# Performance work log

Hardware: AMD Instinct MI355X
Metric: run time of the kernel (lower is better)

Reference implementation:

```python
import jax, jax.numpy as jnp
import numpy as np

N_NODES = 100000
N_EDGES = 1600000
IN_CH = 128
HID = 64
HEADS = 2
OUT_CH = 2
EDGE_DIM = 3
NEG_SLOPE = 0.2
EPS = 1e-16  # PyG softmax denominator epsilon


def gat_conv(x, edge_index, edge_attr, W, We, att_src, att_dst, att_edge, bias, heads, out_ch, concat):
    """Faithful PyG GATConv (edge_dim enabled, eval mode, add_self_loops handled by caller=False here
    since the repo passes raw edge_index; PyG default add_self_loops=True is intentionally mirrored below)."""
    N = x.shape[0]
    src, dst = edge_index[0], edge_index[1]
    H, C = heads, out_ch
    h = (x @ W).reshape(N, H, C)                    # [N,H,C] node projections
    e = (edge_attr @ We).reshape(-1, H, C)          # [E,H,C] edge projections
    a_src = jnp.sum(h * att_src, axis=-1)           # [N,H]
    a_dst = jnp.sum(h * att_dst, axis=-1)           # [N,H]
    alpha = a_src[src] + a_dst[dst] + jnp.sum(e * att_edge, axis=-1)  # [E,H]
    alpha = jax.nn.leaky_relu(alpha, NEG_SLOPE)
    # segment softmax over incoming edges of each dst node
    amax = jax.ops.segment_max(alpha, dst, num_segments=N)            # [N,H]
    amax = jnp.where(jnp.isfinite(amax), amax, 0.0)
    alpha = jnp.exp(alpha - amax[dst])
    denom = jax.ops.segment_sum(alpha, dst, num_segments=N)           # [N,H]
    alpha = alpha / (denom[dst] + EPS)
    msg = h[src] * alpha[:, :, None]                                  # [E,H,C]
    out = jax.ops.segment_sum(msg, dst, num_segments=N)               # [N,H,C]
    if concat:
        out = out.reshape(N, H * C)
    else:
        out = out.mean(axis=1)
    return out + bias


def add_self_loops(edge_index, edge_attr, n):
    loops = jnp.arange(n, dtype=edge_index.dtype)
    ei = jnp.concatenate([edge_index, jnp.stack([loops, loops])], axis=1)
    ea = jnp.concatenate([edge_attr, jnp.zeros((n, edge_attr.shape[1]), edge_attr.dtype)], axis=0)
    return ei, ea


def setup_inputs() -> dict:
    key = jax.random.key(0)
    ks = jax.random.split(key, 16)
    s = 0.1
    x = jax.random.normal(ks[0], (N_NODES, IN_CH), jnp.float32)
    edge_index = jax.random.randint(ks[1], (2, N_EDGES), 0, N_NODES, jnp.int64 if jax.config.jax_enable_x64 else jnp.int32)
    edge_feat = jax.random.normal(ks[2], (N_EDGES, EDGE_DIM), jnp.float32)
    HC = HEADS * HID
    return {
        "x": x, "edge_index": edge_index, "edge_feat": edge_feat,
        "W1": jax.random.normal(ks[3], (IN_CH, HC), jnp.float32) * s,
        "We1": jax.random.normal(ks[4], (EDGE_DIM, HC), jnp.float32) * s,
        "as1": jax.random.normal(ks[5], (1, HEADS, HID), jnp.float32) * s,
        "ad1": jax.random.normal(ks[6], (1, HEADS, HID), jnp.float32) * s,
        "ae1": jax.random.normal(ks[7], (1, HEADS, HID), jnp.float32) * s,
        "b1": jnp.zeros((HC,), jnp.float32),
        "W2": jax.random.normal(ks[8], (HC, OUT_CH), jnp.float32) * s,
        "We2": jax.random.normal(ks[9], (EDGE_DIM, OUT_CH), jnp.float32) * s,
        "as2": jax.random.normal(ks[10], (1, 1, OUT_CH), jnp.float32) * s,
        "ad2": jax.random.normal(ks[11], (1, 1, OUT_CH), jnp.float32) * s,
        "ae2": jax.random.normal(ks[12], (1, 1, OUT_CH), jnp.float32) * s,
        "b2": jnp.zeros((OUT_CH,), jnp.float32),
    }


def reference(x, edge_index, edge_feat, W1, We1, as1, ad1, ae1, b1, W2, We2, as2, ad2, ae2, b2):
    # eval mode: F.dropout is identity
    ei, ea = add_self_loops(edge_index, edge_feat, x.shape[0])  # PyG GATConv default add_self_loops=True
    h = gat_conv(x, ei, ea, W1, We1, as1, ad1, ae1, b1, HEADS, HID, concat=True)
    h = jax.nn.elu(h)
    out = gat_conv(h, ei, ea, W2, We2, as2, ad2, ae2, b2, 1, OUT_CH, concat=False)
    return out
```

## Files before the change

### kernel.cpp

```cpp
#include <hip/hip_runtime.h>
#include <hip/hip_bf16.h>

#define NN 100000
#define NE 1600000
#define NEG_SLOPE 0.2f
#define GEPS 1e-16f
#define WSHIFT 4.0f

#define HB 32
#define EB (NE / HB)
#define HPASS 4
#define HBIN 25000
#define HBW (HBIN / 2)

typedef __attribute__((ext_vector_type(8))) short short8;
typedef __attribute__((ext_vector_type(4))) float f32x4;
typedef __attribute__((ext_vector_type(2))) _Float16 h2v;

__device__ __forceinline__ unsigned short f2b(float f) {
  unsigned u = __float_as_uint(f);
  u += 0x7fffu + ((u >> 16) & 1u);
  return (unsigned short)(u >> 16);
}
__device__ __forceinline__ unsigned short f2h(float f) {
  _Float16 h = (_Float16)f;
  return __builtin_bit_cast(unsigned short, h);
}
__device__ __forceinline__ unsigned pkh2(float lo, float hi) {
  return (unsigned)f2h(lo) | ((unsigned)f2h(hi) << 16);
}
__device__ __forceinline__ float dot2h(unsigned a, unsigned b, float c) {
  return __builtin_amdgcn_fdot2(__builtin_bit_cast(h2v, a), __builtin_bit_cast(h2v, b), c, false);
}
__device__ __forceinline__ unsigned permb(unsigned s0, unsigned s1, int sel) {
  return __builtin_amdgcn_perm(s0, s1, sel);
}
#define HSEL_LO 0x05040100
#define HSEL_HI 0x07060302
#define ONE2    0x3C003C00u

__global__ void k_prep(const float* __restrict__ We1, const float* __restrict__ ae1,
                       const float* __restrict__ We2, const float* __restrict__ ae2,
                       const float* __restrict__ W1, const float* __restrict__ as1,
                       const float* __restrict__ ad1,
                       float* __restrict__ q, float4* __restrict__ pq) {
  int t = threadIdx.x;
  if (t < 6) {
    int d = t >> 1, hh = t & 1;
    float s = 0.f;
    for (int c = 0; c < 64; ++c) s += We1[d * 128 + hh * 64 + c] * ae1[hh * 64 + c];
    q[t] = s;
  } else if (t < 9) {
    int d = t - 6;
    q[8 + d] = We2[d * 2 + 0] * ae2[0] + We2[d * 2 + 1] * ae2[1];
  }
  if (t < 128) {
    float s0 = 0.f, s1 = 0.f, d0 = 0.f, d1 = 0.f;
    for (int c = 0; c < 64; ++c) {
      float w0 = W1[t * 128 + c], w1 = W1[t * 128 + 64 + c];
      s0 += w0 * as1[c];      s1 += w1 * as1[64 + c];
      d0 += w0 * ad1[c];      d1 += w1 * ad1[64 + c];
    }
    pq[t] = make_float4(s0, s1, d0, d1);
  }
}

__global__ __launch_bounds__(512, 4) void k_gemm(const float* __restrict__ x,
                                                 const float* __restrict__ W,
                                                 const float4* __restrict__ pq,
                                                 unsigned short* __restrict__ h1b,
                                                 float* __restrict__ a1s,
                                                 float* __restrict__ a1d) {
  __shared__ unsigned short xa[128 * 128];
  __shared__ unsigned short wt[128 * 128];
  int t = threadIdx.x;
  int row0 = blockIdx.x * 128;

  {
    int kr = t >> 2, n0 = (t & 3) * 32;
    const float* wp = &W[kr * 128 + n0];
    int cb = kr >> 3, klo = kr & 7;
#pragma unroll
    for (int j = 0; j < 8; ++j) {
      float4 v = *(const float4*)&wp[j * 4];
      int n = n0 + j * 4;
      wt[(n + 0) * 128 + ((cb ^ ((n + 0) & 15)) * 8) + klo] = f2b(v.x);
      wt[(n + 1) * 128 + ((cb ^ ((n + 1) & 15)) * 8) + klo] = f2b(v.y);
      wt[(n + 2) * 128 + ((cb ^ ((n + 2) & 15)) * 8) + klo] = f2b(v.z);
      wt[(n + 3) * 128 + ((cb ^ ((n + 3) & 15)) * 8) + klo] = f2b(v.w);
    }
  }
  {
    int lrow = t >> 2, qq = t & 3;
    int grow = row0 + lrow; if (grow >= NN) grow = NN - 1;
    const float* xp = &x[(size_t)grow * 128 + qq * 32];
    const float4* pqp = &pq[qq * 32];
    float ps0 = 0.f, ps1 = 0.f, pd0 = 0.f, pd1 = 0.f;
    int sw = lrow & 15;
#pragma unroll
    for (int j = 0; j < 4; ++j) {
      float4 u = *(const float4*)&xp[j * 8];
      float4 v = *(const float4*)&xp[j * 8 + 4];
      float xs[8] = {u.x, u.y, u.z, u.w, v.x, v.y, v.z, v.w};
      short8 sv;
#pragma unroll
      for (int e = 0; e < 8; ++e) {
        float4 pv = pqp[j * 8 + e];
        ps0 += xs[e] * pv.x; ps1 += xs[e] * pv.y;
        pd0 += xs[e] * pv.z; pd1 += xs[e] * pv.w;
        sv[e] = (short)f2b(xs[e]);
      }
      int c = qq * 4 + j;
      *(short8*)&xa[lrow * 128 + ((c ^ sw) * 8)] = sv;
    }
    ps0 += __shfl_xor(ps0, 1); ps0 += __shfl_xor(ps0, 2);
    ps1 += __shfl_xor(ps1, 1); ps1 += __shfl_xor(ps1, 2);
    pd0 += __shfl_xor(pd0, 1); pd0 += __shfl_xor(pd0, 2);
    pd1 += __shfl_xor(pd1, 1); pd1 += __shfl_xor(pd1, 2);
    if (qq == 0) {
      *(float2*)&a1s[grow * 2] = make_float2(ps0, ps1);
      *(float2*)&a1d[grow * 2] = make_float2(pd0, pd1);
    }
  }
  __syncthreads();

  int lane = t & 63, w = t >> 6;
  int m = lane & 15, quad = lane >> 4;
  int wm = (w & 1) * 64, wn = (w >> 1) * 32;
  f32x4 acc[4][2];
#pragma unroll
  for (int mi = 0; mi < 4; ++mi)
#pragma unroll
    for (int ni = 0; ni < 2; ++ni) acc[mi][ni] = (f32x4)(0.f);

#pragma unroll
  for (int kk = 0; kk < 4; ++kk) {
    int c = kk * 4 + quad;
    int co = (c ^ m) * 8;
    short8 a[4], b[2];
#pragma unroll
    for (int mi = 0; mi < 4; ++mi)
      a[mi] = *(const short8*)&xa[(wm + mi * 16 + m) * 128 + co];
#pragma unroll
    for (int ni = 0; ni < 2; ++ni)
      b[ni] = *(const short8*)&wt[(wn + ni * 16 + m) * 128 + co];
#pragma unroll
    for (int mi = 0; mi < 4; ++mi)
#pragma unroll
      for (int ni = 0; ni < 2; ++ni)
        acc[mi][ni] = __builtin_amdgcn_mfma_f32_16x16x32_bf16(a[mi], b[ni], acc[mi][ni], 0, 0, 0);
  }
#pragma unroll
  for (int mi = 0; mi < 4; ++mi)
#pragma unroll
    for (int r = 0; r < 4; ++r) {
      int grow = row0 + wm + mi * 16 + quad * 4 + r;
      if (grow >= NN) grow = NN - 1;
#pragma unroll
      for (int ni = 0; ni < 2; ++ni)
        h1b[(size_t)grow * 128 + wn + ni * 16 + m] = f2h(acc[mi][ni][r]);
    }
}

__global__ __launch_bounds__(1024) void k_hist(const int* __restrict__ ei,
                                               unsigned short* __restrict__ off16,
                                               unsigned short* __restrict__ rank) {
  __shared__ unsigned cnt[HBW];
  int b = blockIdx.x >> 2;
  int pass = blockIdx.x & 3;
  int base = pass * HBIN;
  int t = threadIdx.x;
  for (int i = t; i < HBW; i += 1024) cnt[i] = 0;
  __syncthreads();
  const int* dsts = &ei[NE + b * EB];
  for (int i = t * 4; i < EB; i += 4096) {
    int4 d = *(const int4*)&dsts[i];
    int dv[4] = {d.x, d.y, d.z, d.w};
#pragma unroll
    for (int j = 0; j < 4; ++j) {
      int rel = dv[j] - base;
      if ((unsigned)rel < (unsigned)HBIN) {
        unsigned sh = (unsigned)(rel & 1) << 4;
        unsigned old = atomicAdd(&cnt[rel >> 1], 1u << sh);
        rank[b * EB + i + j] = (unsigned short)((old >> sh) & 0xffffu);
      }
    }
  }
  __syncthreads();
  unsigned short* dp = &off16[(size_t)b * NN + base];
  for (int i = t; i < HBW; i += 1024) *(unsigned*)&dp[i * 2] = cnt[i];
}

__global__ void k_sumdeg(unsigned short* __restrict__ off16, int* __restrict__ deg) {
  int n = blockIdx.x * 256 + threadIdx.x;
  if (n >= NN) return;
  int run = 0;
#pragma unroll
  for (int b = 0; b < HB; ++b) {
    size_t idx = (size_t)b * NN + n;
    int c = off16[idx];
    off16[idx] = (unsigned short)run;
    run += c;
  }
  deg[n] = run;
}

__device__ __forceinline__ int padlen(int d) { return (d + 8) & ~7; }

__global__ void k_scan1(const int* __restrict__ deg, int* __restrict__ bsum) {
  __shared__ int lds[256];
  int t = threadIdx.x;
  int base = blockIdx.x * 1024 + t * 4;
  int s = 0;
  for (int j = 0; j < 4; ++j) { int i = base + j; s += (i < NN) ? padlen(deg[i]) : 0; }
  lds[t] = s; __syncthreads();
  for (int o = 128; o > 0; o >>= 1) { if (t < o) lds[t] += lds[t + o]; __syncthreads(); }
  if (t == 0) bsum[blockIdx.x] = lds[0];
}

__global__ void k_scan2(int* __restrict__ bsum, int nb) {
  __shared__ int lds[128];
  int t = threadIdx.x;
  int v = (t < nb) ? bsum[t] : 0;
  lds[t] = v; __syncthreads();
  for (int o = 1; o < 128; o <<= 1) {
    int u = (t >= o) ? lds[t - o] : 0;
    __syncthreads();
    lds[t] += u;
    __syncthreads();
  }
  if (t < nb) bsum[t] = lds[t] - v;
}

__global__ void k_scan3(const int* __restrict__ deg, const int* __restrict__ bbase,
                        const float* __restrict__ a1s, const float* __restrict__ a1d,
                        int* __restrict__ rowptr, float4* __restrict__ cpk) {
  __shared__ int lds[256];
  int t = threadIdx.x;
  int base = blockIdx.x * 1024 + t * 4;
  int v[4]; int s = 0;
  for (int j = 0; j < 4; ++j) { int i = base + j; v[j] = (i < NN) ? padlen(deg[i]) : 0; s += v[j]; }
  lds[t] = s; __syncthreads();
  for (int o = 1; o < 256; o <<= 1) {
    int u = (t >= o) ? lds[t - o] : 0;
    __syncthreads();
    lds[t] += u;
    __syncthreads();
  }
  int excl = lds[t] - s + bbase[blockIdx.x];
  for (int j = 0; j < 4; ++j) {
    int i = base + j;
    if (i <= NN) rowptr[i] = excl;
    if (i < NN) {
      float al0 = a1s[i * 2] + a1d[i * 2];
      float al1 = a1s[i * 2 + 1] + a1d[i * 2 + 1];
      al0 = al0 > 0.f ? al0 : NEG_SLOPE * al0;
      al1 = al1 > 0.f ? al1 : NEG_SLOPE * al1;
      float4 pk;
      pk.x = __uint_as_float(pkh2(__expf(al0 - WSHIFT), __expf(al1 - WSHIFT)));
      pk.y = 0.f; pk.z = __int_as_float(i); pk.w = 0.f;
      cpk[excl] = pk;
      float4 pad;
      pad.x = 0.f; pad.y = -1e30f; pad.z = __int_as_float(i); pad.w = 0.f;
      for (int k = 1 + deg[i]; k < v[j]; ++k) cpk[excl + k] = pad;
    }
    excl += v[j];
  }
}

__global__ void k_scatter(const int* __restrict__ ei, const float* __restrict__ ef,
                          const float* __restrict__ a1s, const float* __restrict__ a1d,
                          const float* __restrict__ q, const int* __restrict__ rowptr,
                          const unsigned short* __restrict__ rank,
                          const unsigned short* __restrict__ off16,
                          float4* __restrict__ cpk) {
  int t4 = blockIdx.x * 256 + threadIdx.x;
  if (t4 >= NE / 4) return;
  int e0 = t4 * 4;
  int hb = e0 / EB;
  const unsigned short* offp = &off16[(size_t)hb * NN];
  int4 ss = *(const int4*)&ei[e0];
  int4 dd = *(const int4*)&ei[NE + e0];
  ushort4 rk = *(const ushort4*)&rank[e0];
  float4 fA = *(const float4*)&ef[e0 * 3];
  float4 fB = *(const float4*)&ef[e0 * 3 + 4];
  float4 fC = *(const float4*)&ef[e0 * 3 + 8];
  float f[4][3] = {{fA.x, fA.y, fA.z}, {fA.w, fB.x, fB.y},
                   {fB.z, fB.w, fC.x}, {fC.y, fC.z, fC.w}};
  int src[4] = {ss.x, ss.y, ss.z, ss.w};
  int dst[4] = {dd.x, dd.y, dd.z, dd.w};
  int rnk[4] = {rk.x, rk.y, rk.z, rk.w};
#pragma unroll
  for (int j = 0; j < 4; ++j) {
    float e0h = f[j][0] * q[0] + f[j][1] * q[2] + f[j][2] * q[4];
    float e1h = f[j][0] * q[1] + f[j][1] * q[3] + f[j][2] * q[5];
    float ez  = f[j][0] * q[8] + f[j][1] * q[9] + f[j][2] * q[10];
    float al0 = a1s[src[j] * 2] + a1d[dst[j] * 2] + e0h;
    float al1 = a1s[src[j] * 2 + 1] + a1d[dst[j] * 2 + 1] + e1h;
    al0 = al0 > 0.f ? al0 : NEG_SLOPE * al0;
    al1 = al1 > 0.f ? al1 : NEG_SLOPE * al1;
    int pos = rowptr[dst[j]] + 1 + (int)offp[dst[j]] + rnk[j];
    float4 pk;
    pk.x = __uint_as_float(pkh2(__expf(al0 - WSHIFT), __expf(al1 - WSHIFT)));
    pk.y = ez; pk.z = __int_as_float(src[j]); pk.w = 0.f;
    cpk[pos] = pk;
  }
}

__global__ __launch_bounds__(256) void k_agg1(const unsigned short* __restrict__ h1b,
                                              const int* __restrict__ rowptr,
                                              const float4* __restrict__ cpk,
                                              const float* __restrict__ b1,
                                              const float* __restrict__ W2,
                                              const float* __restrict__ as2,
                                              const float* __restrict__ ad2,
                                              float4* __restrict__ nd) {
  int n = (int)((blockIdx.x * 256 + threadIdx.x) >> 6);
  int lane = threadIdx.x & 63;
  if (n >= NN) return;
  int s0 = rowptr[n], s1 = rowptr[n + 1];
  int g = lane >> 4;
  int lp = lane & 15;
  int wsel = (lp >= 8) ? HSEL_HI : HSEL_LO;

  float acc[8];
#pragma unroll
  for (int j = 0; j < 8; ++j) acc[j] = 0.f;
  float den = 0.f;

  int i = s0;
  for (; i + 16 <= s1; i += 16) {
    float4 pA = cpk[i + g], pB = cpk[i + 4 + g], pC = cpk[i + 8 + g], pD = cpk[i + 12 + g];
    uint4 vA = *((const uint4*)(h1b + ((size_t)__float_as_int(pA.z) << 7)) + lp);
    uint4 vB = *((const uint4*)(h1b + ((size_t)__float_as_int(pB.z) << 7)) + lp);
    uint4 vC = *((const uint4*)(h1b + ((size_t)__float_as_int(pC.z) << 7)) + lp);
    uint4 vD = *((const uint4*)(h1b + ((size_t)__float_as_int(pD.z) << 7)) + lp);
    unsigned wAB = permb(__float_as_uint(pB.x), __float_as_uint(pA.x), wsel);
    unsigned wCD = permb(__float_as_uint(pD.x), __float_as_uint(pC.x), wsel);
    den = dot2h(wAB, ONE2, den);
    den = dot2h(wCD, ONE2, den);
    acc[0] = dot2h(permb(vB.x, vA.x, HSEL_LO), wAB, acc[0]);
    acc[1] = dot2h(permb(vB.x, vA.x, HSEL_HI), wAB, acc[1]);
    acc[2] = dot2h(permb(vB.y, vA.y, HSEL_LO), wAB, acc[2]);
    acc[3] = dot2h(permb(vB.y, vA.y, HSEL_HI), wAB, acc[3]);
    acc[4] = dot2h(permb(vB.z, vA.z, HSEL_LO), wAB, acc[4]);
    acc[5] = dot2h(permb(vB.z, vA.z, HSEL_HI), wAB, acc[5]);
    acc[6] = dot2h(permb(vB.w, vA.w, HSEL_LO), wAB, acc[6]);
    acc[7] = dot2h(permb(vB.w, vA.w, HSEL_HI), wAB, acc[7]);
    acc[0] = dot2h(permb(vD.x, vC.x, HSEL_LO), wCD, acc[0]);
    acc[1] = dot2h(permb(vD.x, vC.x, HSEL_HI), wCD, acc[1]);
    acc[2] = dot2h(permb(vD.y, vC.y, HSEL_LO), wCD, acc[2]);
    acc[3] = dot2h(permb(vD.y, vC.y, HSEL_HI), wCD, acc[3]);
    acc[4] = dot2h(permb(vD.z, vC.z, HSEL_LO), wCD, acc[4]);
    acc[5] = dot2h(permb(vD.z, vC.z, HSEL_HI), wCD, acc[5]);
    acc[6] = dot2h(permb(vD.w, vC.w, HSEL_LO), wCD, acc[6]);
    acc[7] = dot2h(permb(vD.w, vC.w, HSEL_HI), wCD, acc[7]);
  }
  if (i < s1) {
    float4 pA = cpk[i + g], pB = cpk[i + 4 + g];
    uint4 vA = *((const uint4*)(h1b + ((size_t)__float_as_int(pA.z) << 7)) + lp);
    uint4 vB = *((const uint4*)(h1b + ((size_t)__float_as_int(pB.z) << 7)) + lp);
    unsigned wAB = permb(__float_as_uint(pB.x), __float_as_uint(pA.x), wsel);
    den = dot2h(wAB, ONE2, den);
    acc[0] = dot2h(permb(vB.x, vA.x, HSEL_LO), wAB, acc[0]);
    acc[1] = dot2h(permb(vB.x, vA.x, HSEL_HI), wAB, acc[1]);
    acc[2] = dot2h(permb(vB.y, vA.y, HSEL_LO), wAB, acc[2]);
    acc[3] = dot2h(permb(vB.y, vA.y, HSEL_HI), wAB, acc[3]);
    acc[4] = dot2h(permb(vB.z, vA.z, HSEL_LO), wAB, acc[4]);
    acc[5] = dot2h(permb(vB.z, vA.z, HSEL_HI), wAB, acc[5]);
    acc[6] = dot2h(permb(vB.w, vA.w, HSEL_LO), wAB, acc[6]);
    acc[7] = dot2h(permb(vB.w, vA.w, HSEL_HI), wAB, acc[7]);
  }
#pragma unroll
  for (int o = 16; o <= 32; o <<= 1) {
    den += __shfl_xor(den, o);
#pragma unroll
    for (int j = 0; j < 8; ++j) acc[j] += __shfl_xor(acc[j], o);
  }
  float4 bA = *(const float4*)&b1[lp * 8];
  float4 bB = *(const float4*)&b1[lp * 8 + 4];
  float bb[8] = {bA.x, bA.y, bA.z, bA.w, bB.x, bB.y, bB.z, bB.w};
  float inv = 1.f / (den + GEPS);
  float r[8];
#pragma unroll
  for (int j = 0; j < 8; ++j) {
    float v = acc[j] * inv + bb[j];
    r[j] = v > 0.f ? v : __expf(v) - 1.f;
  }
  float4 wA = *(const float4*)&W2[lp * 16];
  float4 wB = *(const float4*)&W2[lp * 16 + 4];
  float4 wC = *(const float4*)&W2[lp * 16 + 8];
  float4 wD = *(const float4*)&W2[lp * 16 + 12];
  float p20 = r[0] * wA.x + r[1] * wA.z + r[2] * wB.x + r[3] * wB.z
            + r[4] * wC.x + r[5] * wC.z + r[6] * wD.x + r[7] * wD.z;
  float p21 = r[0] * wA.y + r[1] * wA.w + r[2] * wB.y + r[3] * wB.w
            + r[4] * wC.y + r[5] * wC.w + r[6] * wD.y + r[7] * wD.w;
#pragma unroll
  for (int o = 1; o <= 8; o <<= 1) { p20 += __shfl_xor(p20, o); p21 += __shfl_xor(p21, o); }
  if (lane == 0) {
    float4 v;
    v.x = p20; v.y = p21;
    v.z = p20 * as2[0] + p21 * as2[1];
    v.w = p20 * ad2[0] + p21 * ad2[1];
    nd[n] = v;
  }
}

__global__ __launch_bounds__(256) void k_agg2(const int* __restrict__ rowptr,
                                              const float4* __restrict__ cpk,
                                              const float4* __restrict__ nd,
                                              const float* __restrict__ b2,
                                              float* __restrict__ out) {
  int wid = (int)((blockIdx.x * 256 + threadIdx.x) >> 6);
  int lane = threadIdx.x & 63;
  int g = lane >> 4, lp = lane & 15;
  int n = wid * 4 + g;
  if (n >= NN) return;
  int s0 = rowptr[n], s1 = rowptr[n + 1];
  float adn = nd[n].w;
  float den = 0.f, acc0 = 0.f, acc1 = 0.f;
  for (int i = s0 + lp; i < s1; i += 16) {
    float4 pk = cpk[i];
    int s = __float_as_int(pk.z);
    float4 ns = nd[s];
    float v = ns.z + adn + pk.y;
    v = v > 0.f ? v : NEG_SLOPE * v;
    float p = __expf(v);
    den += p;
    acc0 += p * ns.x;
    acc1 += p * ns.y;
  }
#pragma unroll
  for (int o = 1; o <= 8; o <<= 1) {
    den += __shfl_xor(den, o);
    acc0 += __shfl_xor(acc0, o);
    acc1 += __shfl_xor(acc1, o);
  }
  if (lp == 0) {
    float2 r;
    r.x = acc0 / (den + GEPS) + b2[0];
    r.y = acc1 / (den + GEPS) + b2[1];
    *(float2*)&out[n * 2] = r;
  }
}

extern "C" void kernel_launch(void* const* d_in, const int* in_sizes, int n_in,
                              void* d_out, int out_size, void* d_ws, size_t ws_size,
                              hipStream_t stream) {
  (void)in_sizes; (void)n_in; (void)out_size; (void)ws_size;
  const float* x   = (const float*)d_in[0];
  const int*   ei  = (const int*)d_in[1];
  const float* ef  = (const float*)d_in[2];
  const float* W1  = (const float*)d_in[3];
  const float* We1 = (const float*)d_in[4];
  const float* as1 = (const float*)d_in[5];
  const float* ad1 = (const float*)d_in[6];
  const float* ae1 = (const float*)d_in[7];
  const float* b1  = (const float*)d_in[8];
  const float* W2  = (const float*)d_in[9];
  const float* We2 = (const float*)d_in[10];
  const float* as2 = (const float*)d_in[11];
  const float* ad2 = (const float*)d_in[12];
  const float* ae2 = (const float*)d_in[13];
  const float* b2  = (const float*)d_in[14];
  float* out = (float*)d_out;

  char* w = (char*)d_ws;
  auto alloc = [&](size_t bytes) -> char* {
    char* p = w; w += (bytes + 255) & ~(size_t)255; return p;
  };
  unsigned short* h1b = (unsigned short*)alloc((size_t)NN * 128 * 2);
  float*  a1s    = (float*)alloc((size_t)NN * 2 * 4);
  float*  a1d    = (float*)alloc((size_t)NN * 2 * 4);
  float4* nd     = (float4*)alloc((size_t)NN * 16);
  float*  q      = (float*)alloc(64);
  float4* pq     = (float4*)alloc(128 * 16);
  int*    deg    = (int*)alloc((size_t)NN * 4);
  int*    rowptr = (int*)alloc((size_t)(NN + 1) * 4);
  unsigned short* rank  = (unsigned short*)alloc((size_t)NE * 2);
  unsigned short* off16 = (unsigned short*)alloc((size_t)HB * NN * 2);
  int*    bsum   = (int*)alloc(128 * 4);
  float4* cpk    = (float4*)alloc(((size_t)NE + 8 * NN) * 16);

  const int NB_SCAN = (NN + 1023) / 1024;

  hipLaunchKernelGGL(k_prep, dim3(1), dim3(128), 0, stream,
                     We1, ae1, We2, ae2, W1, as1, ad1, q, pq);
  hipLaunchKernelGGL(k_gemm, dim3((NN + 127) / 128), dim3(512), 0, stream,
                     x, W1, pq, h1b, a1s, a1d);
  hipLaunchKernelGGL(k_hist, dim3(HB * HPASS), dim3(1024), 0, stream, ei, off16, rank);
  hipLaunchKernelGGL(k_sumdeg, dim3((NN + 255) / 256), dim3(256), 0, stream, off16, deg);
  hipLaunchKernelGGL(k_scan1, dim3(NB_SCAN), dim3(256), 0, stream, deg, bsum);
  hipLaunchKernelGGL(k_scan2, dim3(1), dim3(128), 0, stream, bsum, NB_SCAN);
  hipLaunchKernelGGL(k_scan3, dim3(NB_SCAN), dim3(256), 0, stream,
                     deg, bsum, a1s, a1d, rowptr, cpk);
  hipLaunchKernelGGL(k_scatter, dim3((NE / 4 + 255) / 256), dim3(256), 0, stream,
                     ei, ef, a1s, a1d, q, rowptr, rank, off16, cpk);
  hipLaunchKernelGGL(k_agg1, dim3((NN * 64 + 255) / 256), dim3(256), 0, stream,
                     h1b, rowptr, cpk, b1, W2, as2, ad2, nd);
  hipLaunchKernelGGL(k_agg2, dim3(((NN + 3) / 4 * 64 + 255) / 256), dim3(256), 0, stream,
                     rowptr, cpk, nd, b2, out);
}
```

Baseline: 347.8 us.

## Scatter edge permutation then build compact CSR payload in a sequential pass

The scatter step now writes only a 4-byte edge index into the padded CSR order. A new k_build kernel walks that order sequentially and computes attention weights into an 8-byte (weight, src) array plus a separate edge-logit array. This replaces the 16-byte random scatter writes with small scattered writes followed by coalesced gathers, and shrinks the payload k_agg1 reads per edge from 16 to 8 bytes. It adds one kernel launch and random reads of ei/ef/a1s/a1d in the build pass, and reuses the rank/off16 buffer memory for the edge-logit array.

```diff
diff --git a/kernel.cpp b/kernel.cpp
--- a/kernel.cpp
+++ b/kernel.cpp
@@ -12,6 +12,10 @@
 #define HPASS 4
 #define HBIN 25000
 #define HBW (HBIN / 2)
+#define CAPS (NE + 8 * NN)
+
+#define PM_PAD  0xFFFFFFFFu
+#define PM_SELF 0x40000000u
 
 typedef __attribute__((ext_vector_type(8))) short short8;
 typedef __attribute__((ext_vector_type(4))) float f32x4;
@@ -233,8 +237,7 @@
 }
 
 __global__ void k_scan3(const int* __restrict__ deg, const int* __restrict__ bbase,
-                        const float* __restrict__ a1s, const float* __restrict__ a1d,
-                        int* __restrict__ rowptr, float4* __restrict__ cpk) {
+                        int* __restrict__ rowptr, unsigned* __restrict__ perm) {
   __shared__ int lds[256];
   int t = threadIdx.x;
   int base = blockIdx.x * 1024 + t * 4;
@@ -252,64 +255,91 @@
     int i = base + j;
     if (i <= NN) rowptr[i] = excl;
     if (i < NN) {
-      float al0 = a1s[i * 2] + a1d[i * 2];
-      float al1 = a1s[i * 2 + 1] + a1d[i * 2 + 1];
-      al0 = al0 > 0.f ? al0 : NEG_SLOPE * al0;
-      al1 = al1 > 0.f ? al1 : NEG_SLOPE * al1;
-      float4 pk;
-      pk.x = __uint_as_float(pkh2(__expf(al0 - WSHIFT), __expf(al1 - WSHIFT)));
-      pk.y = 0.f; pk.z = __int_as_float(i); pk.w = 0.f;
-      cpk[excl] = pk;
-      float4 pad;
-      pad.x = 0.f; pad.y = -1e30f; pad.z = __int_as_float(i); pad.w = 0.f;
-      for (int k = 1 + deg[i]; k < v[j]; ++k) cpk[excl + k] = pad;
+      perm[excl] = PM_SELF | (unsigned)i;
+      for (int k = 1 + deg[i]; k < v[j]; ++k) perm[excl + k] = PM_PAD;
     }
     excl += v[j];
   }
 }
 
-__global__ void k_scatter(const int* __restrict__ ei, const float* __restrict__ ef,
-                          const float* __restrict__ a1s, const float* __restrict__ a1d,
-                          const float* __restrict__ q, const int* __restrict__ rowptr,
-                          const unsigned short* __restrict__ rank,
-                          const unsigned short* __restrict__ off16,
-                          float4* __restrict__ cpk) {
+__global__ void k_pscat(const int* __restrict__ ei, const int* __restrict__ rowptr,
+                        const unsigned short* __restrict__ rank,
+                        const unsigned short* __restrict__ off16,
+                        unsigned* __restrict__ perm) {
   int t4 = blockIdx.x * 256 + threadIdx.x;
   if (t4 >= NE / 4) return;
   int e0 = t4 * 4;
   int hb = e0 / EB;
   const unsigned short* offp = &off16[(size_t)hb * NN];
-  int4 ss = *(const int4*)&ei[e0];
   int4 dd = *(const int4*)&ei[NE + e0];
   ushort4 rk = *(const ushort4*)&rank[e0];
-  float4 fA = *(const float4*)&ef[e0 * 3];
-  float4 fB = *(const float4*)&ef[e0 * 3 + 4];
-  float4 fC = *(const float4*)&ef[e0 * 3 + 8];
-  float f[4][3] = {{fA.x, fA.y, fA.z}, {fA.w, fB.x, fB.y},
-                   {fB.z, fB.w, fC.x}, {fC.y, fC.z, fC.w}};
-  int src[4] = {ss.x, ss.y, ss.z, ss.w};
   int dst[4] = {dd.x, dd.y, dd.z, dd.w};
   int rnk[4] = {rk.x, rk.y, rk.z, rk.w};
 #pragma unroll
   for (int j = 0; j < 4; ++j) {
-    float e0h = f[j][0] * q[0] + f[j][1] * q[2] + f[j][2] * q[4];
-    float e1h = f[j][0] * q[1] + f[j][1] * q[3] + f[j][2] * q[5];
-    float ez  = f[j][0] * q[8] + f[j][1] * q[9] + f[j][2] * q[10];
-    float al0 = a1s[src[j] * 2] + a1d[dst[j] * 2] + e0h;
-    float al1 = a1s[src[j] * 2 + 1] + a1d[dst[j] * 2 + 1] + e1h;
-    al0 = al0 > 0.f ? al0 : NEG_SLOPE * al0;
-    al1 = al1 > 0.f ? al1 : NEG_SLOPE * al1;
     int pos = rowptr[dst[j]] + 1 + (int)offp[dst[j]] + rnk[j];
-    float4 pk;
-    pk.x = __uint_as_float(pkh2(__expf(al0 - WSHIFT), __expf(al1 - WSHIFT)));
-    pk.y = ez; pk.z = __int_as_float(src[j]); pk.w = 0.f;
-    cpk[pos] = pk;
-  }
+    perm[pos] = (unsigned)(e0 + j);
+  }
+}
+
+__global__ __launch_bounds__(256) void k_build(const int* __restrict__ ei,
+                                               const float* __restrict__ ef,
+                                               const float* __restrict__ a1s,
+                                               const float* __restrict__ a1d,
+                                               const float* __restrict__ q,
+                                               const int* __restrict__ rowptr,
+                                               const unsigned* __restrict__ perm,
+                                               float2* __restrict__ cpk1,
+                                               float* __restrict__ ez) {
+  int total = rowptr[NN];
+  int i4 = (blockIdx.x * 256 + threadIdx.x) * 4;
+  if (i4 >= total) return;
+  uint4 pv = *(const uint4*)&perm[i4];
+  float q0 = q[0], q1 = q[1], q2 = q[2], q3 = q[3], q4 = q[4], q5 = q[5];
+  float q8 = q[8], q9 = q[9], q10 = q[10];
+  unsigned vv[4] = {pv.x, pv.y, pv.z, pv.w};
+  float o1[8], o2[4];
+#pragma unroll
+  for (int j = 0; j < 4; ++j) {
+    unsigned v = vv[j];
+    float w01b, ezv; int sidx;
+    if (v == PM_PAD) {
+      w01b = 0.f; ezv = -1e30f; sidx = 0;
+    } else {
+      float al0, al1;
+      if (v & PM_SELF) {
+        int n = (int)(v & 0x3FFFFFFFu);
+        sidx = n;
+        float2 s = *(const float2*)&a1s[n * 2];
+        float2 d = *(const float2*)&a1d[n * 2];
+        al0 = s.x + d.x; al1 = s.y + d.y; ezv = 0.f;
+      } else {
+        int e = (int)v;
+        int src = ei[e], dst = ei[NE + e];
+        sidx = src;
+        float f0 = ef[e * 3], f1 = ef[e * 3 + 1], f2 = ef[e * 3 + 2];
+        float2 s = *(const float2*)&a1s[src * 2];
+        float2 d = *(const float2*)&a1d[dst * 2];
+        al0 = s.x + d.x + f0 * q0 + f1 * q2 + f2 * q4;
+        al1 = s.y + d.y + f0 * q1 + f1 * q3 + f2 * q5;
+        ezv = f0 * q8 + f1 * q9 + f2 * q10;
+      }
+      al0 = al0 > 0.f ? al0 : NEG_SLOPE * al0;
+      al1 = al1 > 0.f ? al1 : NEG_SLOPE * al1;
+      w01b = __uint_as_float(pkh2(__expf(al0 - WSHIFT), __expf(al1 - WSHIFT)));
+    }
+    o1[j * 2] = w01b; o1[j * 2 + 1] = __int_as_float(sidx);
+    o2[j] = ezv;
+  }
+  float4* c1 = (float4*)&cpk1[i4];
+  c1[0] = make_float4(o1[0], o1[1], o1[2], o1[3]);
+  c1[1] = make_float4(o1[4], o1[5], o1[6], o1[7]);
+  *(float4*)&ez[i4] = make_float4(o2[0], o2[1], o2[2], o2[3]);
 }
 
 __global__ __launch_bounds__(256) void k_agg1(const unsigned short* __restrict__ h1b,
                                               const int* __restrict__ rowptr,
-                                              const float4* __restrict__ cpk,
+                                              const float2* __restrict__ cpk1,
                                               const float* __restrict__ b1,
                                               const float* __restrict__ W2,
                                               const float* __restrict__ as2,
@@ -330,13 +360,15 @@
 
   int i = s0;
   for (; i + 16 <= s1; i += 16) {
-    float4 pA = cpk[i + g], pB = cpk[i + 4 + g], pC = cpk[i + 8 + g], pD = cpk[i + 12 + g];
-    uint4 vA = *((const uint4*)(h1b + ((size_t)__float_as_int(pA.z) << 7)) + lp);
-    uint4 vB = *((const uint4*)(h1b + ((size_t)__float_as_int(pB.z) << 7)) + lp);
-    uint4 vC = *((const uint4*)(h1b + ((size_t)__float_as_int(pC.z) << 7)) + lp);
-    uint4 vD = *((const uint4*)(h1b + ((size_t)__float_as_int(pD.z) << 7)) + lp);
-    unsigned wAB = permb(__float_as_uint(pB.x), __float_as_uint(pA.x), wsel);
-    unsigned wCD = permb(__float_as_uint(pD.x), __float_as_uint(pC.x), wsel);
+    const float4* pp = (const float4*)(cpk1 + i + 4 * g);
+    float4 p01 = pp[0];
+    float4 p23 = pp[1];
+    uint4 vA = *((const uint4*)(h1b + ((size_t)__float_as_int(p01.y) << 7)) + lp);
+    uint4 vB = *((const uint4*)(h1b + ((size_t)__float_as_int(p01.w) << 7)) + lp);
+    uint4 vC = *((const uint4*)(h1b + ((size_t)__float_as_int(p23.y) << 7)) + lp);
+    uint4 vD = *((const uint4*)(h1b + ((size_t)__float_as_int(p23.w) << 7)) + lp);
+    unsigned wAB = permb(__float_as_uint(p01.z), __float_as_uint(p01.x), wsel);
+    unsigned wCD = permb(__float_as_uint(p23.z), __float_as_uint(p23.x), wsel);
     den = dot2h(wAB, ONE2, den);
     den = dot2h(wCD, ONE2, den);
     acc[0] = dot2h(permb(vB.x, vA.x, HSEL_LO), wAB, acc[0]);
@@ -357,10 +389,10 @@
     acc[7] = dot2h(permb(vD.w, vC.w, HSEL_HI), wCD, acc[7]);
   }
   if (i < s1) {
-    float4 pA = cpk[i + g], pB = cpk[i + 4 + g];
-    uint4 vA = *((const uint4*)(h1b + ((size_t)__float_as_int(pA.z) << 7)) + lp);
-    uint4 vB = *((const uint4*)(h1b + ((size_t)__float_as_int(pB.z) << 7)) + lp);
-    unsigned wAB = permb(__float_as_uint(pB.x), __float_as_uint(pA.x), wsel);
+    float4 p = *(const float4*)(cpk1 + i + 2 * g);
+    uint4 vA = *((const uint4*)(h1b + ((size_t)__float_as_int(p.y) << 7)) + lp);
+    uint4 vB = *((const uint4*)(h1b + ((size_t)__float_as_int(p.w) << 7)) + lp);
+    unsigned wAB = permb(__float_as_uint(p.z), __float_as_uint(p.x), wsel);
     den = dot2h(wAB, ONE2, den);
     acc[0] = dot2h(permb(vB.x, vA.x, HSEL_LO), wAB, acc[0]);
     acc[1] = dot2h(permb(vB.x, vA.x, HSEL_HI), wAB, acc[1]);
@@ -407,7 +439,8 @@
 }
 
 __global__ __launch_bounds__(256) void k_agg2(const int* __restrict__ rowptr,
-                                              const float4* __restrict__ cpk,
+                                              const float2* __restrict__ cpk1,
+                                              const float* __restrict__ ez,
                                               const float4* __restrict__ nd,
                                               const float* __restrict__ b2,
                                               float* __restrict__ out) {
@@ -420,10 +453,11 @@
   float adn = nd[n].w;
   float den = 0.f, acc0 = 0.f, acc1 = 0.f;
   for (int i = s0 + lp; i < s1; i += 16) {
-    float4 pk = cpk[i];
-    int s = __float_as_int(pk.z);
+    float2 pk = cpk1[i];
+    float ezv = ez[i];
+    int s = __float_as_int(pk.y);
     float4 ns = nd[s];
-    float v = ns.z + adn + pk.y;
+    float v = ns.z + adn + ezv;
     v = v > 0.f ? v : NEG_SLOPE * v;
     float p = __expf(v);
     den += p;
@@ -477,10 +511,13 @@
   float4* pq     = (float4*)alloc(128 * 16);
   int*    deg    = (int*)alloc((size_t)NN * 4);
   int*    rowptr = (int*)alloc((size_t)(NN + 1) * 4);
-  unsigned short* rank  = (unsigned short*)alloc((size_t)NE * 2);
-  unsigned short* off16 = (unsigned short*)alloc((size_t)HB * NN * 2);
   int*    bsum   = (int*)alloc(128 * 4);
-  float4* cpk    = (float4*)alloc(((size_t)NE + 8 * NN) * 16);
+  char*   csr_u  = alloc((size_t)CAPS * 4);
+  unsigned short* rank  = (unsigned short*)csr_u;
+  unsigned short* off16 = (unsigned short*)(csr_u + (size_t)NE * 2);
+  float*  ezb    = (float*)csr_u;
+  unsigned* perm = (unsigned*)alloc((size_t)CAPS * 4);
+  float2* cpk1   = (float2*)alloc((size_t)CAPS * 8);
 
   const int NB_SCAN = (NN + 1023) / 1024;
 
@@ -493,11 +530,13 @@
   hipLaunchKernelGGL(k_scan1, dim3(NB_SCAN), dim3(256), 0, stream, deg, bsum);
   hipLaunchKernelGGL(k_scan2, dim3(1), dim3(128), 0, stream, bsum, NB_SCAN);
   hipLaunchKernelGGL(k_scan3, dim3(NB_SCAN), dim3(256), 0, stream,
-                     deg, bsum, a1s, a1d, rowptr, cpk);
-  hipLaunchKernelGGL(k_scatter, dim3((NE / 4 + 255) / 256), dim3(256), 0, stream,
-                     ei, ef, a1s, a1d, q, rowptr, rank, off16, cpk);
+                     deg, bsum, rowptr, perm);
+  hipLaunchKernelGGL(k_pscat, dim3((NE / 4 + 255) / 256), dim3(256), 0, stream,
+                     ei, rowptr, rank, off16, perm);
+  hipLaunchKernelGGL(k_build, dim3((CAPS / 4 + 255) / 256), dim3(256), 0, stream,
+                     ei, ef, a1s, a1d, q, rowptr, perm, cpk1, ezb);
   hipLaunchKernelGGL(k_agg1, dim3((NN * 64 + 255) / 256), dim3(256), 0, stream,
-                     h1b, rowptr, cpk, b1, W2, as2, ad2, nd);
+                     h1b, rowptr, cpk1, b1, W2, as2, ad2, nd);
   hipLaunchKernelGGL(k_agg2, dim3(((NN + 3) / 4 * 64 + 255) / 256), dim3(256), 0, stream,
-                     rowptr, cpk, nd, b2, out);
-}
+                     rowptr, cpk1, ezb, nd, b2, out);
+}
```

Result: slower. 396.0 us (+13.9%).

## Split packed CSR edge records into 8-byte weight/src array plus fp16 edge-logit array

Applied to the files above, without the earlier changes.

Replaces the 16-byte per-edge record (weights, edge logit, src, unused pad) with an 8-byte float2 array holding the packed fp16 weights and the source index, plus a separate fp16 array for the layer-2 edge logit. The first aggregation now reads four edges' weight and source data as two 16-byte loads instead of four, and the scatter and scan write fewer bytes. This cuts edge-list memory traffic in the scatter and both aggregation kernels. In exchange the edge logit is stored in fp16, and padding slots now get a -60000 logit instead of -1e30, which adds a small precision and range risk.

```diff
diff --git a/kernel.cpp b/kernel.cpp
--- a/kernel.cpp
+++ b/kernel.cpp
@@ -12,6 +12,7 @@
 #define HPASS 4
 #define HBIN 25000
 #define HBW (HBIN / 2)
+#define CAPS ((size_t)(NE + 8 * NN))
 
 typedef __attribute__((ext_vector_type(8))) short short8;
 typedef __attribute__((ext_vector_type(4))) float f32x4;
@@ -26,6 +27,9 @@
   _Float16 h = (_Float16)f;
   return __builtin_bit_cast(unsigned short, h);
 }
+__device__ __forceinline__ float h2f(unsigned short u) {
+  return (float)__builtin_bit_cast(_Float16, u);
+}
 __device__ __forceinline__ unsigned pkh2(float lo, float hi) {
   return (unsigned)f2h(lo) | ((unsigned)f2h(hi) << 16);
 }
@@ -38,6 +42,7 @@
 #define HSEL_LO 0x05040100
 #define HSEL_HI 0x07060302
 #define ONE2    0x3C003C00u
+#define EZPAD   (-60000.0f)
 
 __global__ void k_prep(const float* __restrict__ We1, const float* __restrict__ ae1,
                        const float* __restrict__ We2, const float* __restrict__ ae2,
@@ -234,7 +239,8 @@
 
 __global__ void k_scan3(const int* __restrict__ deg, const int* __restrict__ bbase,
                         const float* __restrict__ a1s, const float* __restrict__ a1d,
-                        int* __restrict__ rowptr, float4* __restrict__ cpk) {
+                        int* __restrict__ rowptr, float2* __restrict__ cpk1,
+                        unsigned short* __restrict__ ezh) {
   __shared__ int lds[256];
   int t = threadIdx.x;
   int base = blockIdx.x * 1024 + t * 4;
@@ -248,6 +254,7 @@
     __syncthreads();
   }
   int excl = lds[t] - s + bbase[blockIdx.x];
+  unsigned short ezpad = f2h(EZPAD);
   for (int j = 0; j < 4; ++j) {
     int i = base + j;
     if (i <= NN) rowptr[i] = excl;
@@ -256,13 +263,12 @@
       float al1 = a1s[i * 2 + 1] + a1d[i * 2 + 1];
       al0 = al0 > 0.f ? al0 : NEG_SLOPE * al0;
       al1 = al1 > 0.f ? al1 : NEG_SLOPE * al1;
-      float4 pk;
-      pk.x = __uint_as_float(pkh2(__expf(al0 - WSHIFT), __expf(al1 - WSHIFT)));
-      pk.y = 0.f; pk.z = __int_as_float(i); pk.w = 0.f;
-      cpk[excl] = pk;
-      float4 pad;
-      pad.x = 0.f; pad.y = -1e30f; pad.z = __int_as_float(i); pad.w = 0.f;
-      for (int k = 1 + deg[i]; k < v[j]; ++k) cpk[excl + k] = pad;
+      cpk1[excl] = make_float2(
+          __uint_as_float(pkh2(__expf(al0 - WSHIFT), __expf(al1 - WSHIFT))),
+          __int_as_float(i));
+      ezh[excl] = 0;
+      float2 pad = make_float2(0.f, __int_as_float(i));
+      for (int k = 1 + deg[i]; k < v[j]; ++k) { cpk1[excl + k] = pad; ezh[excl + k] = ezpad; }
     }
     excl += v[j];
   }
@@ -273,7 +279,7 @@
                           const float* __restrict__ q, const int* __restrict__ rowptr,
                           const unsigned short* __restrict__ rank,
                           const unsigned short* __restrict__ off16,
-                          float4* __restrict__ cpk) {
+                          float2* __restrict__ cpk1, unsigned short* __restrict__ ezh) {
   int t4 = blockIdx.x * 256 + threadIdx.x;
   if (t4 >= NE / 4) return;
   int e0 = t4 * 4;
@@ -300,16 +306,16 @@
     al0 = al0 > 0.f ? al0 : NEG_SLOPE * al0;
     al1 = al1 > 0.f ? al1 : NEG_SLOPE * al1;
     int pos = rowptr[dst[j]] + 1 + (int)offp[dst[j]] + rnk[j];
-    float4 pk;
-    pk.x = __uint_as_float(pkh2(__expf(al0 - WSHIFT), __expf(al1 - WSHIFT)));
-    pk.y = ez; pk.z = __int_as_float(src[j]); pk.w = 0.f;
-    cpk[pos] = pk;
+    cpk1[pos] = make_float2(
+        __uint_as_float(pkh2(__expf(al0 - WSHIFT), __expf(al1 - WSHIFT))),
+        __int_as_float(src[j]));
+    ezh[pos] = f2h(ez);
   }
 }
 
 __global__ __launch_bounds__(256) void k_agg1(const unsigned short* __restrict__ h1b,
                                               const int* __restrict__ rowptr,
-                                              const float4* __restrict__ cpk,
+                                              const float2* __restrict__ cpk1,
                                               const float* __restrict__ b1,
                                               const float* __restrict__ W2,
                                               const float* __restrict__ as2,
@@ -330,13 +336,15 @@
 
   int i = s0;
   for (; i + 16 <= s1; i += 16) {
-    float4 pA = cpk[i + g], pB = cpk[i + 4 + g], pC = cpk[i + 8 + g], pD = cpk[i + 12 + g];
-    uint4 vA = *((const uint4*)(h1b + ((size_t)__float_as_int(pA.z) << 7)) + lp);
-    uint4 vB = *((const uint4*)(h1b + ((size_t)__float_as_int(pB.z) << 7)) + lp);
-    uint4 vC = *((const uint4*)(h1b + ((size_t)__float_as_int(pC.z) << 7)) + lp);
-    uint4 vD = *((const uint4*)(h1b + ((size_t)__float_as_int(pD.z) << 7)) + lp);
-    unsigned wAB = permb(__float_as_uint(pB.x), __float_as_uint(pA.x), wsel);
-    unsigned wCD = permb(__float_as_uint(pD.x), __float_as_uint(pC.x), wsel);
+    const float4* pp = (const float4*)(cpk1 + i + 4 * g);
+    float4 p01 = pp[0];
+    float4 p23 = pp[1];
+    uint4 vA = *((const uint4*)(h1b + ((size_t)__float_as_int(p01.y) << 7)) + lp);
+    uint4 vB = *((const uint4*)(h1b + ((size_t)__float_as_int(p01.w) << 7)) + lp);
+    uint4 vC = *((const uint4*)(h1b + ((size_t)__float_as_int(p23.y) << 7)) + lp);
+    uint4 vD = *((const uint4*)(h1b + ((size_t)__float_as_int(p23.w) << 7)) + lp);
+    unsigned wAB = permb(__float_as_uint(p01.z), __float_as_uint(p01.x), wsel);
+    unsigned wCD = permb(__float_as_uint(p23.z), __float_as_uint(p23.x), wsel);
     den = dot2h(wAB, ONE2, den);
     den = dot2h(wCD, ONE2, den);
     acc[0] = dot2h(permb(vB.x, vA.x, HSEL_LO), wAB, acc[0]);
@@ -357,10 +365,10 @@
     acc[7] = dot2h(permb(vD.w, vC.w, HSEL_HI), wCD, acc[7]);
   }
   if (i < s1) {
-    float4 pA = cpk[i + g], pB = cpk[i + 4 + g];
-    uint4 vA = *((const uint4*)(h1b + ((size_t)__float_as_int(pA.z) << 7)) + lp);
-    uint4 vB = *((const uint4*)(h1b + ((size_t)__float_as_int(pB.z) << 7)) + lp);
-    unsigned wAB = permb(__float_as_uint(pB.x), __float_as_uint(pA.x), wsel);
+    float4 p = *(const float4*)(cpk1 + i + 2 * g);
+    uint4 vA = *((const uint4*)(h1b + ((size_t)__float_as_int(p.y) << 7)) + lp);
+    uint4 vB = *((const uint4*)(h1b + ((size_t)__float_as_int(p.w) << 7)) + lp);
+    unsigned wAB = permb(__float_as_uint(p.z), __float_as_uint(p.x), wsel);
     den = dot2h(wAB, ONE2, den);
     acc[0] = dot2h(permb(vB.x, vA.x, HSEL_LO), wAB, acc[0]);
     acc[1] = dot2h(permb(vB.x, vA.x, HSEL_HI), wAB, acc[1]);
@@ -407,7 +415,8 @@
 }
 
 __global__ __launch_bounds__(256) void k_agg2(const int* __restrict__ rowptr,
-                                              const float4* __restrict__ cpk,
+                                              const float2* __restrict__ cpk1,
+                                              const unsigned short* __restrict__ ezh,
                                               const float4* __restrict__ nd,
                                               const float* __restrict__ b2,
                                               float* __restrict__ out) {
@@ -420,10 +429,11 @@
   float adn = nd[n].w;
   float den = 0.f, acc0 = 0.f, acc1 = 0.f;
   for (int i = s0 + lp; i < s1; i += 16) {
-    float4 pk = cpk[i];
-    int s = __float_as_int(pk.z);
+    float2 pk = cpk1[i];
+    float ezv = h2f(ezh[i]);
+    int s = __float_as_int(pk.y);
     float4 ns = nd[s];
-    float v = ns.z + adn + pk.y;
+    float v = ns.z + adn + ezv;
     v = v > 0.f ? v : NEG_SLOPE * v;
     float p = __expf(v);
     den += p;
@@ -480,7 +490,8 @@
   unsigned short* rank  = (unsigned short*)alloc((size_t)NE * 2);
   unsigned short* off16 = (unsigned short*)alloc((size_t)HB * NN * 2);
   int*    bsum   = (int*)alloc(128 * 4);
-  float4* cpk    = (float4*)alloc(((size_t)NE + 8 * NN) * 16);
+  float2* cpk1   = (float2*)alloc(CAPS * 8);
+  unsigned short* ezh = (unsigned short*)alloc(CAPS * 2);
 
   const int NB_SCAN = (NN + 1023) / 1024;
 
@@ -493,11 +504,11 @@
   hipLaunchKernelGGL(k_scan1, dim3(NB_SCAN), dim3(256), 0, stream, deg, bsum);
   hipLaunchKernelGGL(k_scan2, dim3(1), dim3(128), 0, stream, bsum, NB_SCAN);
   hipLaunchKernelGGL(k_scan3, dim3(NB_SCAN), dim3(256), 0, stream,
-                     deg, bsum, a1s, a1d, rowptr, cpk);
+                     deg, bsum, a1s, a1d, rowptr, cpk1, ezh);
   hipLaunchKernelGGL(k_scatter, dim3((NE / 4 + 255) / 256), dim3(256), 0, stream,
-                     ei, ef, a1s, a1d, q, rowptr, rank, off16, cpk);
+                     ei, ef, a1s, a1d, q, rowptr, rank, off16, cpk1, ezh);
   hipLaunchKernelGGL(k_agg1, dim3((NN * 64 + 255) / 256), dim3(256), 0, stream,
-                     h1b, rowptr, cpk, b1, W2, as2, ad2, nd);
+                     h1b, rowptr, cpk1, b1, W2, as2, ad2, nd);
   hipLaunchKernelGGL(k_agg2, dim3(((NN + 3) / 4 * 64 + 255) / 256), dim3(256), 0, stream,
-                     rowptr, cpk, nd, b2, out);
-}
+                     rowptr, cpk1, ezh, nd, b2, out);
+}
```

After: 380.9 us. 1.09x slower.
